# Performance work log

Hardware: AMD Instinct MI355X
Metric: run time of the kernel (lower is better)

The kernel has to match this reference:

```python
import jax, jax.numpy as jnp
import numpy as np

N = 50000          # nodes
E = 1_600_000      # edges (avg degree 32)
D = 128            # in_channels
H = 128            # hidden_channels
B = 4096           # batch_nodes
BETA = 0.5


def setup_inputs() -> dict:
    key = jax.random.key(0)
    ks = jax.random.split(key, 12)
    s = 1.0 / np.sqrt(D)
    inp = {
        "x": jax.random.normal(ks[0], (N, D), jnp.float32),
        "edge_index": jax.random.randint(ks[1], (2, E), 0, N, dtype=jnp.int64),
        "batch_nodes": jax.random.randint(ks[2], (B,), 0, N, dtype=jnp.int64),
        "labels": jax.random.randint(ks[3], (N,), 0, 2, dtype=jnp.int64),
        # GCNConv layer params (weight [in,out], bias [out])
        "W1": jax.random.uniform(ks[4], (D, H), jnp.float32, -s, s),
        "b1": jnp.zeros((H,), jnp.float32),
        "W2": jax.random.uniform(ks[5], (H, H), jnp.float32, -s, s),
        "b2": jnp.zeros((H,), jnp.float32),
        # Bilinear heads: weight [H,H] (out_features=1), scalar bias
        "W_ctx": jax.random.uniform(ks[6], (H, H), jnp.float32, -s, s),
        "b_ctx": jnp.zeros((), jnp.float32),
        "W_loc": jax.random.uniform(ks[7], (H, H), jnp.float32, -s, s),
        "b_loc": jnp.zeros((), jnp.float32),
    }
    return inp


def _gcn_conv(h, W, b, src, dst, n):
    """PyG GCNConv: linear transform, add self-loops, sym-normalized scatter-add."""
    h = h @ W  # [n, out]
    loop = jnp.arange(n, dtype=src.dtype)
    src_f = jnp.concatenate([src, loop])
    dst_f = jnp.concatenate([dst, loop])
    deg = jax.ops.segment_sum(jnp.ones_like(dst_f, dtype=h.dtype), dst_f, num_segments=n)
    dinv = jnp.where(deg > 0, jax.lax.rsqrt(deg), 0.0)
    norm = dinv[src_f] * dinv[dst_f]                      # [E+n]
    msg = h[src_f] * norm[:, None]                        # gather + scale
    out = jax.ops.segment_sum(msg, dst_f, num_segments=n)  # scatter-add
    return out + b


def _bce_logits(z, y):
    # mean(softplus(z) - z*y) == BCEWithLogits
    return jnp.mean(jax.nn.softplus(z) - z * y)


def reference(x, edge_index, batch_nodes, labels, W1, b1, W2, b2, W_ctx, b_ctx, W_loc, b_loc):
    src, dst = edge_index[0], edge_index[1]
    n = x.shape[0]
    layers = [(W1, b1), (W2, b2)]

    # eval mode: dropout is identity
    h = x
    for W, b in layers:
        h = jax.nn.relu(_gcn_conv(h, W, b, src, dst, n))

    gf = h[batch_nodes]                                   # [B, H]
    y = (labels[batch_nodes] == 1).astype(gf.dtype)       # [B]
    pos_cnt = jnp.sum(y)
    neg_cnt = y.shape[0] - pos_cnt
    pos_proto = (y[:, None] * gf).sum(0) / pos_cnt        # [H]

    # context bilinear head: z_i = gf_i^T W_ctx pos_proto + b (neg_sim is dead code in source)
    pos_sim = gf @ (W_ctx @ pos_proto) + b_ctx            # [B]
    ctx_loss = _bce_logits(pos_sim, y)

    # environment view: zero out batch nodes, re-run GCN stack (no dropout in source)
    masked_x = x.at[batch_nodes].set(0.0)
    env_h = masked_x
    for W, b in layers:
        env_h = jax.nn.relu(_gcn_conv(env_h, W, b, src, dst, n))
    env_f = env_h[batch_nodes]                            # [B, H]

    local_sim = jnp.einsum('nd,de,ne->n', env_f, W_loc, gf) + b_loc
    local_loss = _bce_logits(local_sim, 1.0 - y)

    total_loss = BETA * ctx_loss + (1.0 - BETA) * local_loss
    # source's guard: both classes present (true w.h.p. for random labels)
    total_loss = jnp.where((pos_cnt > 0) & (neg_cnt > 0), total_loss, 0.0)
    return gf, total_loss
```

## Files before the change

### kernel.cpp

```cpp
#include <hip/hip_runtime.h>
#include <math.h>

#define HID 128
#define CAP 12288
#define NBUCK_MAX 256
#define EPB 8192

typedef _Float16 h2v __attribute__((ext_vector_type(2)));
typedef _Float16 h8v __attribute__((ext_vector_type(8)));
typedef float f4v __attribute__((ext_vector_type(4)));

static inline int ceil_div(int a, int b) { return (a + b - 1) / b; }


__global__ __launch_bounds__(256) void k_setup(const float* __restrict__ W1, const float* __restrict__ W2,
                                               const float* __restrict__ Wl, _Float16* T1, _Float16* T2,
                                               _Float16* Tl, unsigned int* mask, int* bcur, int mw, int NB) {
    int b = blockIdx.x;
    if (b < 192) {
        int which = b >> 6;
        int idx = (b & 63) * 256 + threadIdx.x;
        int k = idx >> 7, c = idx & 127;
        const float* S = (which == 0) ? W1 : ((which == 1) ? W2 : Wl);
        _Float16* D = (which == 0) ? T1 : ((which == 1) ? T2 : Tl);
        D[c * 128 + k] = (_Float16)S[idx];
    } else {
        int i = (b - 192) * 256 + threadIdx.x;
        if (i < mw) mask[i] = 0u;
        if (i < NB) bcur[i] = i * CAP;
    }
}


__global__ __launch_bounds__(1024) void k_partA(const int* __restrict__ ei, int* __restrict__ bcur,
                                                unsigned int* __restrict__ ebuf,
                                                const int* __restrict__ batch, unsigned int* mask,
                                                int E, int B, int NB, int NBLKE) {
    if ((int)blockIdx.x >= NBLKE) {
        int i = ((int)blockIdx.x - NBLKE) * 1024 + threadIdx.x;
        if (i < B) { int nd = batch[i]; atomicOr(&mask[nd >> 5], 1u << (nd & 31)); }
        return;
    }
    __shared__ int lcnt[NBUCK_MAX];
    __shared__ int sc[NBUCK_MAX];
    __shared__ int lcur[NBUCK_MAX];
    __shared__ int gbase[NBUCK_MAX];
    __shared__ unsigned int se[EPB];
    int tid = threadIdx.x;
    if (tid < NBUCK_MAX) lcnt[tid] = 0;
    __syncthreads();
    int base = blockIdx.x * EPB;
    unsigned int pk[8];
    int bk[8];
#pragma unroll
    for (int j = 0; j < 8; ++j) {
        int e = base + tid + j * 1024;
        if (e < E) {
            int s = ei[e], d = ei[E + e];
            pk[j] = ((unsigned int)s << 8) | (unsigned int)(d & 255);
            bk[j] = d >> 8;
            atomicAdd(&lcnt[bk[j]], 1);
        } else bk[j] = -1;
    }
    __syncthreads();
    if (tid < NBUCK_MAX) sc[tid] = lcnt[tid];
    __syncthreads();
    for (int off = 1; off < NBUCK_MAX; off <<= 1) {
        int v = 0;
        if (tid < NBUCK_MAX && tid >= off) v = sc[tid - off];
        __syncthreads();
        if (tid < NBUCK_MAX) sc[tid] += v;
        __syncthreads();
    }
    if (tid < NBUCK_MAX) {
        int cc = lcnt[tid];
        int lo = sc[tid] - cc;
        lcur[tid] = lo;
        gbase[tid] = cc ? atomicAdd(&bcur[tid], cc) : 0;
    }
    __syncthreads();
#pragma unroll
    for (int j = 0; j < 8; ++j) {
        if (bk[j] >= 0) {
            int r = atomicAdd(&lcur[bk[j]], 1);
            se[r] = pk[j];
        }
    }
    __syncthreads();
    int wid = tid >> 6, lane = tid & 63;
    for (int b = wid; b < NB; b += 16) {
        int cc = lcnt[b];
        int lo = sc[b] - cc;
        int go = gbase[b];
        for (int i = lane; i < cc; i += 64) ebuf[go + i] = se[lo + i];
    }
}


__global__ __launch_bounds__(256) void k_csr(const unsigned int* __restrict__ ebuf, const int* __restrict__ bcur,
                                             const unsigned int* __restrict__ mask, const float* __restrict__ x,
                                             float* __restrict__ sdinv, int* __restrict__ rs,
                                             int* __restrict__ degpk, unsigned int* __restrict__ csr,
                                             _Float16* __restrict__ xs, _Float16* __restrict__ H, int N) {
    __shared__ unsigned int se[CAP];
    __shared__ int deg[256];
    __shared__ int fde[256];
    __shared__ int sc[256];
    __shared__ int cu[256];
    __shared__ int cf[256];
    __shared__ float sda[256];
    int b = blockIdx.x, t = threadIdx.x;
    deg[t] = 0; fde[t] = 0;
    __syncthreads();
    int base = b * CAP;
    int ecnt = bcur[b] - base;
    for (int i = t; i < ecnt; i += 256) {
        unsigned int v = ebuf[base + i];
        int s = v >> 8;
        int fl = (mask[s >> 5] >> (s & 31)) & 1;
        se[i] = ((unsigned int)s << 9) | ((unsigned int)fl << 8) | (v & 255);
        atomicAdd(&deg[v & 255], 1);
        if (fl) atomicAdd(&fde[v & 255], 1);
    }
    __syncthreads();
    int dv = deg[t], fv = fde[t];
    int pv = (dv + 7) & ~7;
    sc[t] = pv;
    __syncthreads();
    for (int off = 1; off < 256; off <<= 1) {
        int v2 = (t >= off) ? sc[t - off] : 0;
        __syncthreads();
        sc[t] += v2;
        __syncthreads();
    }
    int r0 = base + sc[t] - pv;
    cu[t] = r0;
    cf[t] = r0 + (dv - fv);
    int node = b * 256 + t;
    float da = 0.f;
    if (node < N) {
        rs[node] = r0;
        degpk[node] = dv | (fv << 16);
        float di = rsqrtf((float)(dv + 1));
        da = di;
        if ((mask[node >> 5] >> (node & 31)) & 1) di = -di;
        sdinv[node] = di;
    }
    sda[t] = da;
    __syncthreads();
    for (int i = t; i < ecnt; i += 256) {
        unsigned int v = se[i];
        int d8 = v & 255;
        int p = ((v >> 8) & 1) ? atomicAdd(&cf[d8], 1) : atomicAdd(&cu[d8], 1);
        csr[p] = v >> 9;
    }
    if (node < N) {
        for (int j = dv; j < pv; ++j) csr[r0 + j] = (unsigned int)N;
    }
    int nl0 = b * 256;
    int nmax = min(256, N - nl0);
    for (int idx = t; idx < nmax * 16; idx += 256) {
        int nl = idx >> 4, chunk = idx & 15;
        float dda = sda[nl];
        size_t o = (size_t)(nl0 + nl) * HID + chunk * 8;
        float4 a = *(const float4*)&x[o];
        float4 bb = *(const float4*)&x[o + 4];
        h8v v;
        v[0] = (_Float16)(a.x * dda); v[1] = (_Float16)(a.y * dda);
        v[2] = (_Float16)(a.z * dda); v[3] = (_Float16)(a.w * dda);
        v[4] = (_Float16)(bb.x * dda); v[5] = (_Float16)(bb.y * dda);
        v[6] = (_Float16)(bb.z * dda); v[7] = (_Float16)(bb.w * dda);
        *(h8v*)&xs[o] = v;
    }
    if (b == 0) {
        if (t < 16) *(h8v*)&xs[(size_t)N * HID + t * 8] = (h8v){};
        else if (t < 48) *(h8v*)&H[(size_t)2 * N * HID + (t - 16) * 8] = (h8v){};
    }
}


__global__ __launch_bounds__(256) void k_layer1(const _Float16* __restrict__ xs, const int* __restrict__ rs,
                                                const int* __restrict__ degpk, const unsigned int* __restrict__ csr,
                                                const float* __restrict__ sdinv, const _Float16* __restrict__ W1T,
                                                const float* __restrict__ bias, _Float16* __restrict__ H, int N) {
    __shared__ __align__(16) _Float16 sWT[128 * 136];
    __shared__ __align__(16) _Float16 sAgg[32 * 136];
    __shared__ float sbias[128];
    __shared__ float sda[16];
    float* sC = (float*)sWT;

    int tid = threadIdx.x;
    int wave = tid >> 6, lane = tid & 63;
    int grp = lane >> 4, rl = lane & 15;

#pragma unroll
    for (int it = 0; it < 8; ++it) {
        int lin = (it * 256 + tid) * 8;
        int c = lin >> 7, k = lin & 127;
        *(h8v*)&sWT[c * 136 + k] = *(const h8v*)&W1T[lin];
    }
    if (tid < 128) sbias[tid] = bias[tid];
    if (tid < 16) sda[tid] = fabsf(sdinv[blockIdx.x * 16 + tid]);

    int ch = rl * 8;
    int lg = wave * 4 + grp;
    int row = blockIdx.x * 16 + lg;
    bool ok = row < N;
    int p = 0, deg = 0, fd = 0;
    float sd = 0.f;
    h8v hs = {};
    if (ok) {
        p = rs[row];
        int dp = degpk[row];
        deg = dp & 0xffff; fd = dp >> 16;
        sd = sdinv[row];
        hs = *(const h8v*)&xs[(size_t)row * HID + ch];
    }
    int ud = deg - fd;
    int pd = (deg + 7) & ~7;
    int t1 = max(pd, __shfl_xor(pd, 16));
    int m  = max(t1, __shfl_xor(t1, 32));
    float U[8] = {}, F[8] = {};
    for (int i = 0; i < m; i += 16) {
        int id[16];
#pragma unroll
        for (int k = 0; k < 16; ++k) {
            int raw = (int)csr[p + i + k];
            id[k] = (i + k < pd) ? raw : N;
        }
        h8v h[16];
#pragma unroll
        for (int k = 0; k < 16; ++k) h[k] = *(const h8v*)&xs[(size_t)id[k] * HID + ch];
        h8v s0 = (h[0] + h[1]) + (h[2] + h[3]);
        h8v s1 = (h[4] + h[5]) + (h[6] + h[7]);
        h8v s2 = (h[8] + h[9]) + (h[10] + h[11]);
        h8v s3 = (h[12] + h[13]) + (h[14] + h[15]);
        h8v s  = (s0 + s1) + (s2 + s3);
#pragma unroll
        for (int j = 0; j < 8; ++j) U[j] += (float)s[j];
        if (i + 16 > ud) {
#pragma unroll
            for (int k = 0; k < 16; ++k) {
                if (i + k >= ud && i + k < deg) {
#pragma unroll
                    for (int j = 0; j < 8; ++j) F[j] += (float)h[k][j];
                }
            }
        }
    }
    {
        float da = fabsf(sd);
        float keep = (sd < 0.f) ? 0.f : 1.f;
        h8v lo = {}, hi = {};
        if (ok) {
#pragma unroll
            for (int j = 0; j < 8; ++j) {
                float f = (float)hs[j];
                lo[j] = (_Float16)(da * (U[j] + f));
                hi[j] = (_Float16)(da * (U[j] - F[j] + keep * f));
            }
        }
        *(h8v*)&sAgg[(2 * lg) * 136 + ch] = lo;
        *(h8v*)&sAgg[(2 * lg + 1) * 136 + ch] = hi;
    }
    __syncthreads();

    int g = lane >> 4;
    int rowtile = (wave & 1) * 16;
    int colbase = (wave >> 1) * 64;
    f4v acc[4];
#pragma unroll
    for (int cc = 0; cc < 4; ++cc) acc[cc] = (f4v){0.f, 0.f, 0.f, 0.f};
#pragma unroll
    for (int kb = 0; kb < 4; ++kb) {
        int k0 = kb * 32 + g * 8;
        h8v av = *(const h8v*)&sAgg[(rowtile + rl) * 136 + k0];
#pragma unroll
        for (int cc = 0; cc < 4; ++cc) {
            h8v bv = *(const h8v*)&sWT[(colbase + cc * 16 + rl) * 136 + k0];
            acc[cc] = __builtin_amdgcn_mfma_f32_16x16x32_f16(bv, av, acc[cc], 0, 0, 0);
        }
    }
    __syncthreads();

    int lrow = rowtile + rl;
    float dsc = sda[lrow >> 1];
#pragma unroll
    for (int cc = 0; cc < 4; ++cc) {
        f4v v = acc[cc];
        int col = colbase + cc * 16 + g * 4;
#pragma unroll
        for (int i2 = 0; i2 < 4; ++i2) v[i2] = fmaxf(v[i2] + sbias[col + i2], 0.f) * dsc;
        *(f4v*)&sC[lrow * 132 + col] = v;
    }
    __syncthreads();

    int sr = tid >> 3, ck = tid & 7;
    int gRow = blockIdx.x * 32 + sr;
    if (gRow < 2 * N) {
        const float* src = &sC[sr * 132 + ck * 16];
        h8v o0, o1;
#pragma unroll
        for (int j = 0; j < 8; ++j) { o0[j] = (_Float16)src[j]; o1[j] = (_Float16)src[8 + j]; }
        _Float16* dst = &H[(size_t)gRow * HID + ck * 16];
        *(h8v*)&dst[0] = o0;
        *(h8v*)&dst[8] = o1;
    }
}


__global__ __launch_bounds__(256) void k_layer2(const _Float16* __restrict__ H, const int* __restrict__ rs,
                                                const int* __restrict__ degpk, const unsigned int* __restrict__ csr,
                                                const float* __restrict__ sdinv, const int* __restrict__ batch,
                                                const _Float16* __restrict__ W2T, const float* __restrict__ bias,
                                                float* __restrict__ gf, _Float16* __restrict__ envh, int B, int N) {
    __shared__ __align__(16) _Float16 sWT[128 * 136];
    __shared__ __align__(16) _Float16 sAgg[32 * 136];
    __shared__ float sbias[128];
    float* sC = (float*)sWT;

    int tid = threadIdx.x;
    int wave = tid >> 6, lane = tid & 63;
    int grp = lane >> 4, rl = lane & 15;

#pragma unroll
    for (int it = 0; it < 8; ++it) {
        int lin = (it * 256 + tid) * 8;
        int c = lin >> 7, k = lin & 127;
        *(h8v*)&sWT[c * 136 + k] = *(const h8v*)&W2T[lin];
    }
    if (tid < 128) sbias[tid] = bias[tid];

    int ch = rl * 8;
    int lg = wave * 4 + grp;
    int ri = blockIdx.x * 16 + lg;
    bool ok = ri < B;
    int p = 0, deg = 0, row = 0;
    float da = 0.f;
    h8v hn = {}, he = {};
    if (ok) {
        row = batch[ri];
        p = rs[row];
        deg = degpk[row] & 0xffff;
        da = fabsf(sdinv[row]);
        hn = *(const h8v*)&H[(size_t)row * 256 + ch];
        he = *(const h8v*)&H[(size_t)row * 256 + 128 + ch];
    }
    int pd = (deg + 7) & ~7;
    int t1 = max(pd, __shfl_xor(pd, 16));
    int m  = max(t1, __shfl_xor(t1, 32));
    float a[8] = {}, e[8] = {};
    for (int i = 0; i < m; i += 8) {
        int id[8];
#pragma unroll
        for (int k = 0; k < 8; ++k) {
            int raw = (int)csr[p + i + k];
            id[k] = (i + k < pd) ? raw : N;
        }
        h8v xn[8], xe[8];
#pragma unroll
        for (int k = 0; k < 8; ++k) {
            xn[k] = *(const h8v*)&H[(size_t)id[k] * 256 + ch];
            xe[k] = *(const h8v*)&H[(size_t)id[k] * 256 + 128 + ch];
        }
        h8v sn = ((xn[0] + xn[1]) + (xn[2] + xn[3])) + ((xn[4] + xn[5]) + (xn[6] + xn[7]));
        h8v sv = ((xe[0] + xe[1]) + (xe[2] + xe[3])) + ((xe[4] + xe[5]) + (xe[6] + xe[7]));
#pragma unroll
        for (int j = 0; j < 8; ++j) { a[j] += (float)sn[j]; e[j] += (float)sv[j]; }
    }
    {
        h8v lo = {}, hi = {};
        if (ok) {
#pragma unroll
            for (int j = 0; j < 8; ++j) {
                lo[j] = (_Float16)(da * (a[j] + (float)hn[j]));
                hi[j] = (_Float16)(da * (e[j] + (float)he[j]));
            }
        }
        *(h8v*)&sAgg[(2 * lg) * 136 + ch] = lo;
        *(h8v*)&sAgg[(2 * lg + 1) * 136 + ch] = hi;
    }
    __syncthreads();

    int g = lane >> 4;
    int rowtile = (wave & 1) * 16;
    int colbase = (wave >> 1) * 64;
    f4v acc[4];
#pragma unroll
    for (int cc = 0; cc < 4; ++cc) acc[cc] = (f4v){0.f, 0.f, 0.f, 0.f};
#pragma unroll
    for (int kb = 0; kb < 4; ++kb) {
        int k0 = kb * 32 + g * 8;
        h8v av = *(const h8v*)&sAgg[(rowtile + rl) * 136 + k0];
#pragma unroll
        for (int cc = 0; cc < 4; ++cc) {
            h8v bv = *(const h8v*)&sWT[(colbase + cc * 16 + rl) * 136 + k0];
            acc[cc] = __builtin_amdgcn_mfma_f32_16x16x32_f16(bv, av, acc[cc], 0, 0, 0);
        }
    }
    __syncthreads();

    int lrow = rowtile + rl;
#pragma unroll
    for (int cc = 0; cc < 4; ++cc) {
        f4v v = acc[cc];
        int col = colbase + cc * 16 + g * 4;
#pragma unroll
        for (int i2 = 0; i2 < 4; ++i2) v[i2] = fmaxf(v[i2] + sbias[col + i2], 0.f);
        *(f4v*)&sC[lrow * 132 + col] = v;
    }
    __syncthreads();

    int sr = tid >> 3, ck = tid & 7;
    int ri2 = blockIdx.x * 16 + (sr >> 1);
    if (ri2 < B) {
        const float* src = &sC[sr * 132 + ck * 16];
        if ((sr & 1) == 0) {
            float* dst = &gf[(size_t)ri2 * HID + ck * 16];
#pragma unroll
            for (int q = 0; q < 4; ++q) *(float4*)&dst[q * 4] = *(const float4*)&src[q * 4];
        } else {
            h8v o0, o1;
#pragma unroll
            for (int j = 0; j < 8; ++j) { o0[j] = (_Float16)src[j]; o1[j] = (_Float16)src[8 + j]; }
            _Float16* dst = &envh[(size_t)ri2 * HID + ck * 16];
            *(h8v*)&dst[0] = o0;
            *(h8v*)&dst[8] = o1;
        }
    }
}


__global__ __launch_bounds__(256) void k_gemmT(const _Float16* __restrict__ A, const _Float16* __restrict__ WT,
                                               _Float16* __restrict__ outH, int n2) {
    __shared__ __align__(16) char smem[128 * 136 * 2];
    _Float16* sWT = (_Float16*)smem;
    float* sC = (float*)smem;
    int tid = threadIdx.x;
#pragma unroll
    for (int it = 0; it < 8; ++it) {
        int lin = (it * 256 + tid) * 8;
        int c = lin >> 7, k = lin & 127;
        *(h8v*)&sWT[c * 136 + k] = *(const h8v*)&WT[lin];
    }
    __syncthreads();

    int wave = tid >> 6, lane = tid & 63;
    int rl = lane & 15, g = lane >> 4;
    int r = blockIdx.x * 64 + wave * 16 + rl;
    bool rok = r < n2;
    f4v acc[8];
#pragma unroll
    for (int cf = 0; cf < 8; ++cf) acc[cf] = (f4v){0.f, 0.f, 0.f, 0.f};
#pragma unroll
    for (int kb = 0; kb < 4; ++kb) {
        int k0 = kb * 32 + g * 8;
        h8v av = {};
        if (rok) av = *(const h8v*)&A[(size_t)r * HID + k0];
#pragma unroll
        for (int cf = 0; cf < 8; ++cf) {
            h8v bv = *(const h8v*)&sWT[(cf * 16 + rl) * 136 + k0];
            acc[cf] = __builtin_amdgcn_mfma_f32_16x16x32_f16(bv, av, acc[cf], 0, 0, 0);
        }
    }
    __syncthreads();
    int lrow = wave * 16 + rl;
#pragma unroll
    for (int cf = 0; cf < 8; ++cf) {
        *(f4v*)&sC[lrow * 132 + cf * 16 + g * 4] = acc[cf];
    }
    __syncthreads();
    int lr = tid >> 2, seg = tid & 3;
    int R = blockIdx.x * 64 + lr;
    if (R < n2) {
        const float* src = &sC[lr * 132 + seg * 32];
        _Float16* dst = &outH[(size_t)R * HID + seg * 32];
#pragma unroll
        for (int qq = 0; qq < 4; ++qq) {
            h8v o;
#pragma unroll
            for (int j = 0; j < 8; ++j) o[j] = (_Float16)src[qq * 8 + j];
            *(h8v*)&dst[qq * 8] = o;
        }
    }
}


__global__ __launch_bounds__(256) void k_possum(const float* __restrict__ gf, const int* __restrict__ batch,
                                                const int* __restrict__ labels, float* __restrict__ yv,
                                                float* __restrict__ part, float* __restrict__ pos_part) {
    __shared__ float s[256];
    __shared__ float sy[256];
    int t = threadIdx.x;
    int r0 = blockIdx.x * 256;
    int b = r0 + t;
    float y = (labels[batch[b]] == 1) ? 1.f : 0.f;
    yv[b] = y;
    sy[t] = y;
    __syncthreads();
    int ch = t & 127, half = t >> 7;
    float acc = 0.f;
    for (int r = half; r < 256; r += 2) acc += sy[r] * gf[(size_t)(r0 + r) * HID + ch];
    s[t] = acc;
    __syncthreads();
    if (t < 128) part[blockIdx.x * 128 + t] = s[t] + s[t + 128];
    __syncthreads();
    s[t] = sy[t];
    __syncthreads();
    for (int st = 128; st > 0; st >>= 1) {
        if (t < st) s[t] += s[t + st];
        __syncthreads();
    }
    if (t == 0) pos_part[blockIdx.x] = s[0];
}

__global__ __launch_bounds__(128) void k_ctxvec(const float* __restrict__ Wctx, const float* __restrict__ part,
                                                const float* __restrict__ pos_part, float* v, float* pcnt) {
    __shared__ float sproto[128];
    __shared__ float spc;
    int t = threadIdx.x;
    if (t == 0) {
        float pc = 0.f;
        for (int i = 0; i < 16; ++i) pc += pos_part[i];
        spc = pc;
        pcnt[0] = pc;
    }
    float ssum = 0.f;
    for (int i = 0; i < 16; ++i) ssum += part[i * 128 + t];
    __syncthreads();
    sproto[t] = ssum / spc;
    __syncthreads();
    float acc = 0.f;
#pragma unroll 4
    for (int j = 0; j < 128; ++j) acc += Wctx[t * 128 + j] * sproto[j];
    v[t] = acc;
}

__global__ __launch_bounds__(256) void k_heads(const float* __restrict__ gf, const _Float16* __restrict__ T,
                                               const float* __restrict__ v, const float* __restrict__ yv,
                                               const float* __restrict__ bctx, const float* __restrict__ bloc,
                                               float* pA, float* pB, int B) {
    int wave = threadIdx.x >> 6, lane = threadIdx.x & 63;
    int b = blockIdx.x * 4 + wave;
    if (b >= B) return;
    float2 g = *(const float2*)&gf[(size_t)b * HID + lane * 2];
    h2v tt = *(const h2v*)&T[(size_t)b * HID + lane * 2];
    float2 vv = *(const float2*)&v[lane * 2];
    float s1 = g.x * vv.x + g.y * vv.y;
    float s2 = g.x * (float)tt[0] + g.y * (float)tt[1];
    for (int o = 32; o > 0; o >>= 1) {
        s1 += __shfl_xor(s1, o);
        s2 += __shfl_xor(s2, o);
    }
    if (lane == 0) {
        float y = yv[b];
        float z1 = s1 + bctx[0];
        float z2 = s2 + bloc[0];
        pA[b] = fmaxf(z1, 0.f) + log1pf(expf(-fabsf(z1))) - z1 * y;
        pB[b] = fmaxf(z2, 0.f) + log1pf(expf(-fabsf(z2))) - z2 * (1.f - y);
    }
}

__global__ __launch_bounds__(256) void k_final(const float* __restrict__ pA, const float* __restrict__ pB,
                                               const float* __restrict__ pcnt, float* out_loss, int B) {
    __shared__ float s1[256];
    __shared__ float s2[256];
    int t = threadIdx.x;
    float a = 0.f, b2 = 0.f;
    for (int i = t; i < B; i += 256) { a += pA[i]; b2 += pB[i]; }
    s1[t] = a;
    s2[t] = b2;
    __syncthreads();
    for (int st = 128; st > 0; st >>= 1) {
        if (t < st) { s1[t] += s1[t + st]; s2[t] += s2[t + st]; }
        __syncthreads();
    }
    if (t == 0) {
        float pc = pcnt[0];
        float nc = (float)B - pc;
        float total = 0.5f * (s1[0] / (float)B) + 0.5f * (s2[0] / (float)B);
        out_loss[0] = (pc > 0.f && nc > 0.f) ? total : 0.f;
    }
}


extern "C" void kernel_launch(void* const* d_in, const int* in_sizes, int n_in,
                              void* d_out, int out_size, void* d_ws, size_t ws_size,
                              hipStream_t stream) {
    const float* x      = (const float*)d_in[0];
    const int*   ei     = (const int*)d_in[1];
    const int*   batch  = (const int*)d_in[2];
    const int*   labels = (const int*)d_in[3];
    const float* W1     = (const float*)d_in[4];
    const float* b1     = (const float*)d_in[5];
    const float* W2     = (const float*)d_in[6];
    const float* b2     = (const float*)d_in[7];
    const float* Wctx   = (const float*)d_in[8];
    const float* bctx   = (const float*)d_in[9];
    const float* Wloc   = (const float*)d_in[10];
    const float* bloc   = (const float*)d_in[11];

    int N = in_sizes[0] / HID;
    int E = in_sizes[1] / 2;
    int B = in_sizes[2];
    float* out = (float*)d_out;

    char* wsb = (char*)d_ws;
    size_t off = 0;
    auto alloc = [&](size_t bytes) -> char* {
        char* p = wsb + off;
        off += (bytes + 255) & ~(size_t)255;
        return p;
    };
    int NB = ceil_div(N, 256);
    int mw = ceil_div(N, 32);

    _Float16* xs   = (_Float16*)alloc((size_t)(N + 1) * HID * 2);
    _Float16* H    = (_Float16*)alloc((size_t)(2 * N + 2) * HID * 2);
    unsigned int* ebuf = (unsigned int*)alloc((size_t)NB * CAP * 4);
    unsigned int* csr  = (unsigned int*)alloc((size_t)NB * CAP * 4);
    float* sdinv = (float*)alloc((size_t)N * 4);
    int*   rs    = (int*)alloc((size_t)N * 4);
    int*   degpk = (int*)alloc((size_t)N * 4);
    int*   bcur  = (int*)alloc((size_t)NB * 4);
    unsigned int* mask = (unsigned int*)alloc((size_t)mw * 4);
    _Float16* W1T = (_Float16*)alloc(128 * 128 * 2);
    _Float16* W2T = (_Float16*)alloc(128 * 128 * 2);
    _Float16* WlT = (_Float16*)alloc(128 * 128 * 2);
    _Float16* envh  = (_Float16*)alloc((size_t)B * HID * 2);
    _Float16* Tt    = (_Float16*)alloc((size_t)B * HID * 2);
    float* yv   = (float*)alloc((size_t)B * 4);
    float* pos_part = (float*)alloc(64 * 4);
    float* part     = (float*)alloc(16 * 128 * 4);
    float* vvec     = (float*)alloc(128 * 4);
    float* pcnt     = (float*)alloc(256);
    float* pA       = (float*)alloc((size_t)B * 4);
    float* pB       = (float*)alloc((size_t)B * 4);
    (void)ws_size; (void)n_in; (void)out_size;

    int NBLKE = ceil_div(E, EPB);
    int NBLKB = ceil_div(B, 1024);

    k_setup<<<192 + ceil_div(mw, 256), 256, 0, stream>>>(W1, W2, Wloc, W1T, W2T, WlT, mask, bcur, mw, NB);
    k_partA<<<NBLKE + NBLKB, 1024, 0, stream>>>(ei, bcur, ebuf, batch, mask, E, B, NB, NBLKE);
    k_csr<<<NB, 256, 0, stream>>>(ebuf, bcur, mask, x, sdinv, rs, degpk, csr, xs, H, N);

    k_layer1<<<ceil_div(N, 16), 256, 0, stream>>>(xs, rs, degpk, csr, sdinv, W1T, b1, H, N);

    k_layer2<<<ceil_div(B, 16), 256, 0, stream>>>(H, rs, degpk, csr, sdinv, batch, W2T, b2, out, envh, B, N);

    k_gemmT<<<ceil_div(B, 64), 256, 0, stream>>>(envh, WlT, Tt, B);

    k_possum<<<16, 256, 0, stream>>>(out, batch, labels, yv, part, pos_part);
    k_ctxvec<<<1, 128, 0, stream>>>(Wctx, part, pos_part, vvec, pcnt);
    k_heads<<<ceil_div(B, 4), 256, 0, stream>>>(out, Tt, vvec, yv, bctx, bloc, pA, pB, B);
    k_final<<<1, 256, 0, stream>>>(pA, pB, pcnt, out + (size_t)B * HID, B);
}
```

Measured before the change: 176.5 us.

## Fuse tail kernels: positive-sum into layer2, W_loc GEMM with heads, atomic loss reduction

The epilogue of layer2 now computes the labels and accumulates the positive prototype sum and count through atomics, which replaces k_possum. The W_loc GEMM is fused with both bilinear heads and the BCE loss, so the intermediate T matrix and the per-row loss arrays are never written, and k_final shrinks to a scalar combine. The x-to-fp16 cast moves out of k_csr into its own fully parallel elementwise kernel. Together this cuts the tail from seven launches to four at the cost of one extra launch for the cast. It also adds float atomics, which make the summation order nondeterministic.

```diff
diff --git a/kernel.cpp b/kernel.cpp
--- a/kernel.cpp
+++ b/kernel.cpp
@@ -15,19 +15,26 @@
 
 __global__ __launch_bounds__(256) void k_setup(const float* __restrict__ W1, const float* __restrict__ W2,
                                                const float* __restrict__ Wl, _Float16* T1, _Float16* T2,
-                                               _Float16* Tl, unsigned int* mask, int* bcur, int mw, int NB) {
+                                               _Float16* Tl, unsigned int* mask, int* bcur,
+                                               float* part, float* pcnt_raw, float* lsums, int mw, int NB) {
     int b = blockIdx.x;
+    int t = threadIdx.x;
     if (b < 192) {
         int which = b >> 6;
-        int idx = (b & 63) * 256 + threadIdx.x;
+        int idx = (b & 63) * 256 + t;
         int k = idx >> 7, c = idx & 127;
         const float* S = (which == 0) ? W1 : ((which == 1) ? W2 : Wl);
         _Float16* D = (which == 0) ? T1 : ((which == 1) ? T2 : Tl);
         D[c * 128 + k] = (_Float16)S[idx];
     } else {
-        int i = (b - 192) * 256 + threadIdx.x;
+        int i = (b - 192) * 256 + t;
         if (i < mw) mask[i] = 0u;
         if (i < NB) bcur[i] = i * CAP;
+        if (b == 192) {
+            if (t < 128) part[t] = 0.f;
+            else if (t == 128) pcnt_raw[0] = 0.f;
+            else if (t < 131) lsums[t - 129] = 0.f;
+        }
     }
 }
 
@@ -98,17 +105,15 @@
 
 
 __global__ __launch_bounds__(256) void k_csr(const unsigned int* __restrict__ ebuf, const int* __restrict__ bcur,
-                                             const unsigned int* __restrict__ mask, const float* __restrict__ x,
+                                             const unsigned int* __restrict__ mask,
                                              float* __restrict__ sdinv, int* __restrict__ rs,
-                                             int* __restrict__ degpk, unsigned int* __restrict__ csr,
-                                             _Float16* __restrict__ xs, _Float16* __restrict__ H, int N) {
+                                             int* __restrict__ degpk, unsigned int* __restrict__ csr, int N) {
     __shared__ unsigned int se[CAP];
     __shared__ int deg[256];
     __shared__ int fde[256];
     __shared__ int sc[256];
     __shared__ int cu[256];
     __shared__ int cf[256];
-    __shared__ float sda[256];
     int b = blockIdx.x, t = threadIdx.x;
     deg[t] = 0; fde[t] = 0;
     __syncthreads();
@@ -137,16 +142,13 @@
     cu[t] = r0;
     cf[t] = r0 + (dv - fv);
     int node = b * 256 + t;
-    float da = 0.f;
     if (node < N) {
         rs[node] = r0;
         degpk[node] = dv | (fv << 16);
         float di = rsqrtf((float)(dv + 1));
-        da = di;
         if ((mask[node >> 5] >> (node & 31)) & 1) di = -di;
         sdinv[node] = di;
     }
-    sda[t] = da;
     __syncthreads();
     for (int i = t; i < ecnt; i += 256) {
         unsigned int v = se[i];
@@ -157,24 +159,30 @@
     if (node < N) {
         for (int j = dv; j < pv; ++j) csr[r0 + j] = (unsigned int)N;
     }
-    int nl0 = b * 256;
-    int nmax = min(256, N - nl0);
-    for (int idx = t; idx < nmax * 16; idx += 256) {
-        int nl = idx >> 4, chunk = idx & 15;
-        float dda = sda[nl];
-        size_t o = (size_t)(nl0 + nl) * HID + chunk * 8;
+}
+
+
+__global__ __launch_bounds__(256) void k_cast(const float* __restrict__ x, const float* __restrict__ sdinv,
+                                              _Float16* __restrict__ xs, _Float16* __restrict__ H, int N) {
+    int i = blockIdx.x * 256 + threadIdx.x;
+    int nx = N * 16;
+    if (i < nx) {
+        int node = i >> 4;
+        float da = fabsf(sdinv[node]);
+        int o = i * 8;
         float4 a = *(const float4*)&x[o];
-        float4 bb = *(const float4*)&x[o + 4];
+        float4 b = *(const float4*)&x[o + 4];
         h8v v;
-        v[0] = (_Float16)(a.x * dda); v[1] = (_Float16)(a.y * dda);
-        v[2] = (_Float16)(a.z * dda); v[3] = (_Float16)(a.w * dda);
-        v[4] = (_Float16)(bb.x * dda); v[5] = (_Float16)(bb.y * dda);
-        v[6] = (_Float16)(bb.z * dda); v[7] = (_Float16)(bb.w * dda);
+        v[0] = (_Float16)(a.x * da); v[1] = (_Float16)(a.y * da);
+        v[2] = (_Float16)(a.z * da); v[3] = (_Float16)(a.w * da);
+        v[4] = (_Float16)(b.x * da); v[5] = (_Float16)(b.y * da);
+        v[6] = (_Float16)(b.z * da); v[7] = (_Float16)(b.w * da);
         *(h8v*)&xs[o] = v;
-    }
-    if (b == 0) {
-        if (t < 16) *(h8v*)&xs[(size_t)N * HID + t * 8] = (h8v){};
-        else if (t < 48) *(h8v*)&H[(size_t)2 * N * HID + (t - 16) * 8] = (h8v){};
+    } else if (i < nx + 16) {
+        *(h8v*)&xs[(size_t)i * 8] = (h8v){};
+    } else if (i < nx + 16 + 32) {
+        int j = i - (nx + 16);
+        *(h8v*)&H[(size_t)2 * N * HID + j * 8] = (h8v){};
     }
 }
 
@@ -312,11 +320,15 @@
 __global__ __launch_bounds__(256) void k_layer2(const _Float16* __restrict__ H, const int* __restrict__ rs,
                                                 const int* __restrict__ degpk, const unsigned int* __restrict__ csr,
                                                 const float* __restrict__ sdinv, const int* __restrict__ batch,
+                                                const int* __restrict__ labels,
                                                 const _Float16* __restrict__ W2T, const float* __restrict__ bias,
-                                                float* __restrict__ gf, _Float16* __restrict__ envh, int B, int N) {
+                                                float* __restrict__ gf, _Float16* __restrict__ envh,
+                                                float* __restrict__ yv, float* __restrict__ part,
+                                                float* __restrict__ pcnt_raw, int B, int N) {
     __shared__ __align__(16) _Float16 sWT[128 * 136];
     __shared__ __align__(16) _Float16 sAgg[32 * 136];
     __shared__ float sbias[128];
+    __shared__ float sy2[16];
     float* sC = (float*)sWT;
 
     int tid = threadIdx.x;
@@ -428,107 +440,37 @@
             *(h8v*)&dst[8] = o1;
         }
     }
-}
-
-
-__global__ __launch_bounds__(256) void k_gemmT(const _Float16* __restrict__ A, const _Float16* __restrict__ WT,
-                                               _Float16* __restrict__ outH, int n2) {
-    __shared__ __align__(16) char smem[128 * 136 * 2];
-    _Float16* sWT = (_Float16*)smem;
-    float* sC = (float*)smem;
-    int tid = threadIdx.x;
-#pragma unroll
-    for (int it = 0; it < 8; ++it) {
-        int lin = (it * 256 + tid) * 8;
-        int c = lin >> 7, k = lin & 127;
-        *(h8v*)&sWT[c * 136 + k] = *(const h8v*)&WT[lin];
-    }
-    __syncthreads();
-
-    int wave = tid >> 6, lane = tid & 63;
-    int rl = lane & 15, g = lane >> 4;
-    int r = blockIdx.x * 64 + wave * 16 + rl;
-    bool rok = r < n2;
-    f4v acc[8];
-#pragma unroll
-    for (int cf = 0; cf < 8; ++cf) acc[cf] = (f4v){0.f, 0.f, 0.f, 0.f};
-#pragma unroll
-    for (int kb = 0; kb < 4; ++kb) {
-        int k0 = kb * 32 + g * 8;
-        h8v av = {};
-        if (rok) av = *(const h8v*)&A[(size_t)r * HID + k0];
-#pragma unroll
-        for (int cf = 0; cf < 8; ++cf) {
-            h8v bv = *(const h8v*)&sWT[(cf * 16 + rl) * 136 + k0];
-            acc[cf] = __builtin_amdgcn_mfma_f32_16x16x32_f16(bv, av, acc[cf], 0, 0, 0);
-        }
-    }
-    __syncthreads();
-    int lrow = wave * 16 + rl;
-#pragma unroll
-    for (int cf = 0; cf < 8; ++cf) {
-        *(f4v*)&sC[lrow * 132 + cf * 16 + g * 4] = acc[cf];
-    }
-    __syncthreads();
-    int lr = tid >> 2, seg = tid & 3;
-    int R = blockIdx.x * 64 + lr;
-    if (R < n2) {
-        const float* src = &sC[lr * 132 + seg * 32];
-        _Float16* dst = &outH[(size_t)R * HID + seg * 32];
-#pragma unroll
-        for (int qq = 0; qq < 4; ++qq) {
-            h8v o;
-#pragma unroll
-            for (int j = 0; j < 8; ++j) o[j] = (_Float16)src[qq * 8 + j];
-            *(h8v*)&dst[qq * 8] = o;
-        }
-    }
-}
-
-
-__global__ __launch_bounds__(256) void k_possum(const float* __restrict__ gf, const int* __restrict__ batch,
-                                                const int* __restrict__ labels, float* __restrict__ yv,
-                                                float* __restrict__ part, float* __restrict__ pos_part) {
-    __shared__ float s[256];
-    __shared__ float sy[256];
+
+    int rr = blockIdx.x * 16 + tid;
+    if (tid < 16) {
+        float y = 0.f;
+        if (rr < B) {
+            y = (labels[batch[rr]] == 1) ? 1.f : 0.f;
+            yv[rr] = y;
+        }
+        sy2[tid] = y;
+    }
+    __syncthreads();
+    if (tid < 128) {
+        float acc2 = 0.f;
+#pragma unroll
+        for (int r2 = 0; r2 < 16; ++r2) acc2 += sy2[r2] * sC[(2 * r2) * 132 + tid];
+        atomicAdd(&part[tid], acc2);
+    } else if (tid == 128) {
+        float ps = 0.f;
+#pragma unroll
+        for (int r2 = 0; r2 < 16; ++r2) ps += sy2[r2];
+        atomicAdd(&pcnt_raw[0], ps);
+    }
+}
+
+
+__global__ __launch_bounds__(128) void k_ctxvec(const float* __restrict__ Wctx, const float* __restrict__ part,
+                                                const float* __restrict__ pcnt_raw, float* v) {
+    __shared__ float sproto[128];
     int t = threadIdx.x;
-    int r0 = blockIdx.x * 256;
-    int b = r0 + t;
-    float y = (labels[batch[b]] == 1) ? 1.f : 0.f;
-    yv[b] = y;
-    sy[t] = y;
-    __syncthreads();
-    int ch = t & 127, half = t >> 7;
-    float acc = 0.f;
-    for (int r = half; r < 256; r += 2) acc += sy[r] * gf[(size_t)(r0 + r) * HID + ch];
-    s[t] = acc;
-    __syncthreads();
-    if (t < 128) part[blockIdx.x * 128 + t] = s[t] + s[t + 128];
-    __syncthreads();
-    s[t] = sy[t];
-    __syncthreads();
-    for (int st = 128; st > 0; st >>= 1) {
-        if (t < st) s[t] += s[t + st];
-        __syncthreads();
-    }
-    if (t == 0) pos_part[blockIdx.x] = s[0];
-}
-
-__global__ __launch_bounds__(128) void k_ctxvec(const float* __restrict__ Wctx, const float* __restrict__ part,
-                                                const float* __restrict__ pos_part, float* v, float* pcnt) {
-    __shared__ float sproto[128];
-    __shared__ float spc;
-    int t = threadIdx.x;
-    if (t == 0) {
-        float pc = 0.f;
-        for (int i = 0; i < 16; ++i) pc += pos_part[i];
-        spc = pc;
-        pcnt[0] = pc;
-    }
-    float ssum = 0.f;
-    for (int i = 0; i < 16; ++i) ssum += part[i * 128 + t];
-    __syncthreads();
-    sproto[t] = ssum / spc;
+    float pc = pcnt_raw[0];
+    sproto[t] = part[t] / pc;
     __syncthreads();
     float acc = 0.f;
 #pragma unroll 4
@@ -536,49 +478,78 @@
     v[t] = acc;
 }
 
-__global__ __launch_bounds__(256) void k_heads(const float* __restrict__ gf, const _Float16* __restrict__ T,
-                                               const float* __restrict__ v, const float* __restrict__ yv,
-                                               const float* __restrict__ bctx, const float* __restrict__ bloc,
-                                               float* pA, float* pB, int B) {
-    int wave = threadIdx.x >> 6, lane = threadIdx.x & 63;
-    int b = blockIdx.x * 4 + wave;
-    if (b >= B) return;
-    float2 g = *(const float2*)&gf[(size_t)b * HID + lane * 2];
-    h2v tt = *(const h2v*)&T[(size_t)b * HID + lane * 2];
-    float2 vv = *(const float2*)&v[lane * 2];
-    float s1 = g.x * vv.x + g.y * vv.y;
-    float s2 = g.x * (float)tt[0] + g.y * (float)tt[1];
-    for (int o = 32; o > 0; o >>= 1) {
-        s1 += __shfl_xor(s1, o);
-        s2 += __shfl_xor(s2, o);
-    }
-    if (lane == 0) {
-        float y = yv[b];
+
+__global__ __launch_bounds__(256) void k_headsT(const _Float16* __restrict__ envh, const float* __restrict__ gf,
+                                                const _Float16* __restrict__ WlT, const float* __restrict__ v,
+                                                const float* __restrict__ yv, const float* __restrict__ bctx,
+                                                const float* __restrict__ bloc, float* __restrict__ lsums, int B) {
+    __shared__ __align__(16) _Float16 sWT[128 * 136];
+    __shared__ float sv[128];
+    int tid = threadIdx.x;
+#pragma unroll
+    for (int it = 0; it < 8; ++it) {
+        int lin = (it * 256 + tid) * 8;
+        int c = lin >> 7, k = lin & 127;
+        *(h8v*)&sWT[c * 136 + k] = *(const h8v*)&WlT[lin];
+    }
+    if (tid < 128) sv[tid] = v[tid];
+    __syncthreads();
+
+    int wave = tid >> 6, lane = tid & 63;
+    int rl = lane & 15, g = lane >> 4;
+    int r = blockIdx.x * 64 + wave * 16 + rl;
+    bool rok = r < B;
+    f4v acc[8];
+#pragma unroll
+    for (int cf = 0; cf < 8; ++cf) acc[cf] = (f4v){0.f, 0.f, 0.f, 0.f};
+#pragma unroll
+    for (int kb = 0; kb < 4; ++kb) {
+        int k0 = kb * 32 + g * 8;
+        h8v av = {};
+        if (rok) av = *(const h8v*)&envh[(size_t)r * HID + k0];
+#pragma unroll
+        for (int cf = 0; cf < 8; ++cf) {
+            h8v bv = *(const h8v*)&sWT[(cf * 16 + rl) * 136 + k0];
+            acc[cf] = __builtin_amdgcn_mfma_f32_16x16x32_f16(bv, av, acc[cf], 0, 0, 0);
+        }
+    }
+    float s1 = 0.f, s2 = 0.f;
+    if (rok) {
+#pragma unroll
+        for (int cf = 0; cf < 8; ++cf) {
+            int col = cf * 16 + g * 4;
+            float4 gv = *(const float4*)&gf[(size_t)r * HID + col];
+            s2 += acc[cf][0] * gv.x + acc[cf][1] * gv.y + acc[cf][2] * gv.z + acc[cf][3] * gv.w;
+            s1 += sv[col] * gv.x + sv[col + 1] * gv.y + sv[col + 2] * gv.z + sv[col + 3] * gv.w;
+        }
+    }
+    s1 += __shfl_xor(s1, 16); s1 += __shfl_xor(s1, 32);
+    s2 += __shfl_xor(s2, 16); s2 += __shfl_xor(s2, 32);
+    float l1 = 0.f, l2 = 0.f;
+    if (g == 0 && rok) {
+        float y = yv[r];
         float z1 = s1 + bctx[0];
         float z2 = s2 + bloc[0];
-        pA[b] = fmaxf(z1, 0.f) + log1pf(expf(-fabsf(z1))) - z1 * y;
-        pB[b] = fmaxf(z2, 0.f) + log1pf(expf(-fabsf(z2))) - z2 * (1.f - y);
-    }
-}
-
-__global__ __launch_bounds__(256) void k_final(const float* __restrict__ pA, const float* __restrict__ pB,
-                                               const float* __restrict__ pcnt, float* out_loss, int B) {
-    __shared__ float s1[256];
-    __shared__ float s2[256];
-    int t = threadIdx.x;
-    float a = 0.f, b2 = 0.f;
-    for (int i = t; i < B; i += 256) { a += pA[i]; b2 += pB[i]; }
-    s1[t] = a;
-    s2[t] = b2;
-    __syncthreads();
-    for (int st = 128; st > 0; st >>= 1) {
-        if (t < st) { s1[t] += s1[t + st]; s2[t] += s2[t + st]; }
-        __syncthreads();
-    }
-    if (t == 0) {
-        float pc = pcnt[0];
+        l1 = fmaxf(z1, 0.f) + log1pf(expf(-fabsf(z1))) - z1 * y;
+        l2 = fmaxf(z2, 0.f) + log1pf(expf(-fabsf(z2))) - z2 * (1.f - y);
+    }
+#pragma unroll
+    for (int o = 1; o < 64; o <<= 1) {
+        l1 += __shfl_xor(l1, o);
+        l2 += __shfl_xor(l2, o);
+    }
+    if (lane == 0) {
+        atomicAdd(&lsums[0], l1);
+        atomicAdd(&lsums[1], l2);
+    }
+}
+
+__global__ void k_final(const float* __restrict__ lsums, const float* __restrict__ pcnt_raw,
+                        float* out_loss, int B) {
+    if (blockIdx.x == 0 && threadIdx.x == 0) {
+        float pc = pcnt_raw[0];
         float nc = (float)B - pc;
-        float total = 0.5f * (s1[0] / (float)B) + 0.5f * (s2[0] / (float)B);
+        float total = 0.5f * (lsums[0] / (float)B) + 0.5f * (lsums[1] / (float)B);
         out_loss[0] = (pc > 0.f && nc > 0.f) ? total : 0.f;
     }
 }
@@ -628,31 +599,28 @@
     _Float16* W2T = (_Float16*)alloc(128 * 128 * 2);
     _Float16* WlT = (_Float16*)alloc(128 * 128 * 2);
     _Float16* envh  = (_Float16*)alloc((size_t)B * HID * 2);
-    _Float16* Tt    = (_Float16*)alloc((size_t)B * HID * 2);
-    float* yv   = (float*)alloc((size_t)B * 4);
-    float* pos_part = (float*)alloc(64 * 4);
-    float* part     = (float*)alloc(16 * 128 * 4);
-    float* vvec     = (float*)alloc(128 * 4);
-    float* pcnt     = (float*)alloc(256);
-    float* pA       = (float*)alloc((size_t)B * 4);
-    float* pB       = (float*)alloc((size_t)B * 4);
+    float* yv    = (float*)alloc((size_t)B * 4);
+    float* part  = (float*)alloc(128 * 4);
+    float* pcnt_raw = (float*)alloc(256);
+    float* lsums = (float*)alloc(256);
+    float* vvec  = (float*)alloc(128 * 4);
     (void)ws_size; (void)n_in; (void)out_size;
 
     int NBLKE = ceil_div(E, EPB);
     int NBLKB = ceil_div(B, 1024);
 
-    k_setup<<<192 + ceil_div(mw, 256), 256, 0, stream>>>(W1, W2, Wloc, W1T, W2T, WlT, mask, bcur, mw, NB);
+    k_setup<<<192 + ceil_div(mw, 256), 256, 0, stream>>>(W1, W2, Wloc, W1T, W2T, WlT, mask, bcur,
+                                                         part, pcnt_raw, lsums, mw, NB);
     k_partA<<<NBLKE + NBLKB, 1024, 0, stream>>>(ei, bcur, ebuf, batch, mask, E, B, NB, NBLKE);
-    k_csr<<<NB, 256, 0, stream>>>(ebuf, bcur, mask, x, sdinv, rs, degpk, csr, xs, H, N);
+    k_csr<<<NB, 256, 0, stream>>>(ebuf, bcur, mask, sdinv, rs, degpk, csr, N);
+    k_cast<<<ceil_div(N * 16 + 48, 256), 256, 0, stream>>>(x, sdinv, xs, H, N);
 
     k_layer1<<<ceil_div(N, 16), 256, 0, stream>>>(xs, rs, degpk, csr, sdinv, W1T, b1, H, N);
 
-    k_layer2<<<ceil_div(B, 16), 256, 0, stream>>>(H, rs, degpk, csr, sdinv, batch, W2T, b2, out, envh, B, N);
-
-    k_gemmT<<<ceil_div(B, 64), 256, 0, stream>>>(envh, WlT, Tt, B);
-
-    k_possum<<<16, 256, 0, stream>>>(out, batch, labels, yv, part, pos_part);
-    k_ctxvec<<<1, 128, 0, stream>>>(Wctx, part, pos_part, vvec, pcnt);
-    k_heads<<<ceil_div(B, 4), 256, 0, stream>>>(out, Tt, vvec, yv, bctx, bloc, pA, pB, B);
-    k_final<<<1, 256, 0, stream>>>(pA, pB, pcnt, out + (size_t)B * HID, B);
-}
+    k_layer2<<<ceil_div(B, 16), 256, 0, stream>>>(H, rs, degpk, csr, sdinv, batch, labels, W2T, b2,
+                                                  out, envh, yv, part, pcnt_raw, B, N);
+
+    k_ctxvec<<<1, 128, 0, stream>>>(Wctx, part, pcnt_raw, vvec);
+    k_headsT<<<ceil_div(B, 64), 256, 0, stream>>>(envh, out, WlT, vvec, yv, bctx, bloc, lsums, B);
+    k_final<<<1, 1, 0, stream>>>(lsums, pcnt_raw, out + (size_t)B * HID, B);
+}
```

After: 145.8 us. 1.21x faster.
